# Kernel tuning notes

Hardware: AMD Instinct MI355X
Metric: run time of the kernel (lower is better)

The kernel has to match this reference:

```python
import jax, jax.numpy as jnp
import numpy as np

B, N, LAT, H, NL, NH = 1, 512, 128, 256, 3, 4
EMB = H // 4  # atom-type embedding dim = 64
DH = H // NH  # head dim = 64
LN_EPS = 1e-5


def _lin(x, w, b):
    # torch nn.Linear convention: w is (out, in)
    return x @ w.T + b


def _ln(x, s, b):
    m = jnp.mean(x, -1, keepdims=True)
    v = jnp.mean((x - m) ** 2, -1, keepdims=True)
    return (x - m) / jnp.sqrt(v + LN_EPS) * s + b


def setup_inputs() -> dict:
    key = jax.random.key(0)
    ks = iter(jax.random.split(key, 64))
    def w(shape, scale=0.02):
        return (jax.random.normal(next(ks), shape, jnp.float32) * scale).astype(jnp.float32)
    inp = dict(
        z=jax.random.normal(next(ks), (B, N, LAT), jnp.float32),
        z_global=jax.random.normal(next(ks), (B, LAT), jnp.float32),
        atom_types=jax.random.randint(next(ks), (B, N), 0, 4),
        emb=w((4, EMB), 1.0),
        ip_w1=w((H, LAT + EMB)), ip_b1=jnp.zeros(H), ip_w2=w((H, H)), ip_b2=jnp.zeros(H),
        gp_w1=w((H, LAT)), gp_b1=jnp.zeros(H), gp_w2=w((H, H)), gp_b2=jnp.zeros(H),
        tf_wqkv=w((NL, 3 * H, H)), tf_bqkv=jnp.zeros((NL, 3 * H)),
        tf_wo=w((NL, H, H)), tf_bo=jnp.zeros((NL, H)),
        tf_ln1_s=jnp.ones((NL, H)), tf_ln1_b=jnp.zeros((NL, H)),
        tf_w1=w((NL, 4 * H, H)), tf_b1=jnp.zeros((NL, 4 * H)),
        tf_w2=w((NL, H, 4 * H)), tf_b2=jnp.zeros((NL, H)),
        tf_ln2_s=jnp.ones((NL, H)), tf_ln2_b=jnp.zeros((NL, H)),
        dp_w1=w((H, 2 * H)), dp_b1=jnp.zeros(H), dp_w2=w((H, H)), dp_b2=jnp.zeros(H),
        dp_w3=w((1, H)), dp_b3=jnp.zeros(1),
        cp_w1=w((H, H)), cp_b1=jnp.zeros(H), cp_w2=w((3, H)), cp_b2=jnp.zeros(3),
    )
    return inp


def _forward(z, z_global, atom_types, emb,
             ip_w1, ip_b1, ip_w2, ip_b2,
             gp_w1, gp_b1, gp_w2, gp_b2,
             tf_wqkv, tf_bqkv, tf_wo, tf_bo, tf_ln1_s, tf_ln1_b,
             tf_w1, tf_b1, tf_w2, tf_b2, tf_ln2_s, tf_ln2_b,
             dp_w1, dp_b1, dp_w2, dp_b2, dp_w3, dp_b3,
             cp_w1, cp_b1, cp_w2, cp_b2):
    Bs, Ns = z.shape[0], z.shape[1]
    atom_feats = emb[atom_types]                      # (B,N,EMB)
    z_input = jnp.concatenate([z, atom_feats], -1)    # (B,N,LAT+EMB)
    h = _lin(jax.nn.silu(_lin(z_input, ip_w1, ip_b1)), ip_w2, ip_b2)
    g = _lin(jax.nn.silu(_lin(z_global, gp_w1, gp_b1)), gp_w2, gp_b2)
    h = h + g[:, None, :]
    # post-norm TransformerEncoder (relu FFN, eval mode -> no dropout)
    scale = 1.0 / np.sqrt(DH)
    for l in range(NL):
        qkv = _lin(h, tf_wqkv[l], tf_bqkv[l])
        q, k, v = jnp.split(qkv, 3, -1)
        q = q.reshape(Bs, Ns, NH, DH)
        k = k.reshape(Bs, Ns, NH, DH)
        v = v.reshape(Bs, Ns, NH, DH)
        att = jax.nn.softmax(jnp.einsum('bqhd,bkhd->bhqk', q, k) * scale, -1)
        o = jnp.einsum('bhqk,bkhd->bqhd', att, v).reshape(Bs, Ns, H)
        h = _ln(h + _lin(o, tf_wo[l], tf_bo[l]), tf_ln1_s[l], tf_ln1_b[l])
        ff = _lin(jax.nn.relu(_lin(h, tf_w1[l], tf_b1[l])), tf_w2[l], tf_b2[l])
        h = _ln(h + ff, tf_ln2_s[l], tf_ln2_b[l])
    # dist head: Linear(concat(h_i,h_j)) == h_i @ W[:, :H].T + h_j @ W[:, H:].T + b
    # (avoids materializing the (B,N,N,2H) concat; identical math)
    ai = h @ dp_w1[:, :H].T                           # (B,N,H)
    aj = h @ dp_w1[:, H:].T                           # (B,N,H)
    pair = jax.nn.silu(ai[:, :, None, :] + aj[:, None, :, :] + dp_b1)  # (B,N,N,H)
    pair = jax.nn.silu(_lin(pair, dp_w2, dp_b2))
    dist = jax.nn.softplus(_lin(pair, dp_w3, dp_b3))[..., 0]           # (B,N,N)
    dist = (dist + jnp.swapaxes(dist, 1, 2)) * 0.5
    x = _lin(jax.nn.silu(_lin(h, cp_w1, cp_b1)), cp_w2, cp_b2)          # (B,N,3)
    return x, dist


def reference(z, z_global, atom_types, emb,
              ip_w1, ip_b1, ip_w2, ip_b2,
              gp_w1, gp_b1, gp_w2, gp_b2,
              tf_wqkv, tf_bqkv, tf_wo, tf_bo, tf_ln1_s, tf_ln1_b,
              tf_w1, tf_b1, tf_w2, tf_b2, tf_ln2_s, tf_ln2_b,
              dp_w1, dp_b1, dp_w2, dp_b2, dp_w3, dp_b3,
              cp_w1, cp_b1, cp_w2, cp_b2):
    return _forward(z, z_global, atom_types, emb,
                    ip_w1, ip_b1, ip_w2, ip_b2,
                    gp_w1, gp_b1, gp_w2, gp_b2,
                    tf_wqkv, tf_bqkv, tf_wo, tf_bo, tf_ln1_s, tf_ln1_b,
                    tf_w1, tf_b1, tf_w2, tf_b2, tf_ln2_s, tf_ln2_b,
                    dp_w1, dp_b1, dp_w2, dp_b2, dp_w3, dp_b3,
                    cp_w1, cp_b1, cp_w2, cp_b2)
```

## Files before the change

kernel.cpp:

```cpp
#include <hip/hip_runtime.h>
#include <hip/hip_bf16.h>
#include <cstdint>

typedef __bf16 bf16;
typedef __attribute__((ext_vector_type(8))) __bf16 bf16x8;
typedef __attribute__((ext_vector_type(4))) float f32x4;

#define MFMA16(a, b, c) __builtin_amdgcn_mfma_f32_16x16x32_bf16(a, b, c, 0, 0, 0)

__device__ __forceinline__ float fast_rcp(float x) { return __builtin_amdgcn_rcpf(x); }
__device__ __forceinline__ float silu_f(float x) { return x * fast_rcp(1.f + __expf(-x)); }
__device__ __forceinline__ bf16x8 cvt8(float4 a, float4 b) {
  bf16x8 o;
  o[0]=(bf16)a.x; o[1]=(bf16)a.y; o[2]=(bf16)a.z; o[3]=(bf16)a.w;
  o[4]=(bf16)b.x; o[5]=(bf16)b.y; o[6]=(bf16)b.z; o[7]=(bf16)b.w;
  return o;
}

constexpr long WB_IPW1 = 0;
constexpr long WB_IPW2 = 49152;
constexpr long WB_QKV  = 114688;
constexpr long WB_WO   = 704512;
constexpr long WB_W1   = 901120;
constexpr long WB_W2   = 1687552;
constexpr long WB_CPW1 = 2670592;
constexpr long F_ZIN = 5472256;
constexpr long F_G   = F_ZIN + 512L*192*4;
constexpr long F_H   = F_G + 1024;
constexpr long F_QKV = F_H + 512L*256*4;
constexpr long F_S   = F_QKV + 512L*768*4;
constexpr long F_VT  = F_S + 4L*512*512*4;
constexpr long F_O   = F_VT + 4L*64*512*2;
constexpr long F_T1  = F_O + 512L*256*4;
constexpr long O_W2P  = F_T1 + 512L*256*4;
constexpr long O_WDP  = O_W2P + 131072;
constexpr long O_B512 = O_WDP + 262144;

__global__ __launch_bounds__(256) void prep_kernel(
    const float* __restrict__ s_ipw1, const float* __restrict__ s_ipw2,
    const float* __restrict__ s_qkv,  const float* __restrict__ s_wo,
    const float* __restrict__ s_w1,   const float* __restrict__ s_w2,
    const float* __restrict__ s_dpw1, const float* __restrict__ s_dpw2,
    const float* __restrict__ s_cpw1, bf16* __restrict__ dst,
    const float* __restrict__ z, const int* __restrict__ at, const float* __restrict__ emb,
    const float* __restrict__ zg, const float* __restrict__ gw1, const float* __restrict__ gb1,
    const float* __restrict__ gw2, const float* __restrict__ gb2,
    const float* __restrict__ dpb1,
    float* __restrict__ zi, bf16* __restrict__ w2p, bf16* __restrict__ wdp,
    float* __restrict__ g, float* __restrict__ bias512)
{
  __shared__ float zs[128];
  __shared__ float ts[256];
  const int b = blockIdx.x, tid = threadIdx.x;
  if (b < 2672) {
    long v = (long)b * 256 + tid;
    if (v >= 684032) return;
    const float* src; long off;
    if (v < 176128) {
      if (v < 12288)      { src = s_ipw1; off = 0; }
      else if (v < 28672) { src = s_ipw2; off = 12288; }
      else                { src = s_qkv;  off = 28672; }
    } else if (v < 618496) {
      if (v < 225280)      { src = s_wo; off = 176128; }
      else if (v < 421888) { src = s_w1; off = 225280; }
      else                 { src = s_w2; off = 421888; }
    } else {
      if (v < 651264)      { src = s_dpw1; off = 618496; }
      else if (v < 667648) { src = s_dpw2; off = 651264; }
      else                 { src = s_cpw1; off = 667648; }
    }
    long e = (v - off) * 4;
    float4 f = *(const float4*)&src[e];
    bf16* d = dst + off * 4 + e;
    d[0] = (bf16)f.x; d[1] = (bf16)f.y; d[2] = (bf16)f.z; d[3] = (bf16)f.w;
  } else if (b < 3056) {
    int idx = (b - 2672) * 256 + tid;
    int n = idx / 192, c = idx - n * 192;
    zi[idx] = (c < 128) ? z[n * 128 + c] : emb[at[n] * 64 + (c - 128)];
  } else if (b < 3088) {
    int f = (b - 3056) * 256 + tid;
    int l15 = f & 15, kq = (f >> 4) & 3, ks = (f >> 6) & 7, nt = f >> 9;
    int n = nt * 16 + l15, k0 = ks * 32 + kq * 8;
    float4 v0 = *(const float4*)&s_dpw2[n * 256 + k0];
    float4 v1 = *(const float4*)&s_dpw2[n * 256 + k0 + 4];
    *(bf16x8*)&w2p[(long)f * 8] = cvt8(v0, v1);
  } else if (b < 3216) {
    int v = (b - 3088) * 256 + tid;
    int r = v >> 6, c4 = (v & 63) << 2;
    long src = (r < 256) ? ((long)r * 512 + c4) : ((long)(r - 256) * 512 + 256 + c4);
    float4 f = *(const float4*)&s_dpw1[src];
    bf16* d = &wdp[r * 256 + c4];
    d[0]=(bf16)f.x; d[1]=(bf16)f.y; d[2]=(bf16)f.z; d[3]=(bf16)f.w;
  } else if (b == 3216) {
    if (tid < 128) zs[tid] = zg[tid];
    __syncthreads();
    float s = gb1[tid];
    for (int k = 0; k < 128; ++k) s += zs[k] * gw1[tid * 128 + k];
    ts[tid] = silu_f(s);
    __syncthreads();
    float s2 = gb2[tid];
    for (int k = 0; k < 256; ++k) s2 += ts[k] * gw2[tid * 256 + k];
    g[tid] = s2;
  } else {
    bias512[tid] = dpb1[tid];
    bias512[256 + tid] = 0.f;
  }
}

template<int ACT, typename WT>
__global__ __launch_bounds__(256) void gemm_kernel(
    const float* __restrict__ A, int lda, long sA,
    const WT* __restrict__ W, int ldw, long sW,
    const float* __restrict__ bias,
    const float* __restrict__ R, int ldr, long sR,
    float* __restrict__ C, int ldc, long sC, int K)
{
  const int bz = blockIdx.z;
  A += (long)bz * sA;  W += (long)bz * sW;  C += (long)bz * sC;
  if (R) R += (long)bz * sR;
  const int m0 = blockIdx.x * 64, n0 = blockIdx.y * 64;
  __shared__ bf16 As[64][72];
  __shared__ bf16 Ws[64][72];
  const int tid = threadIdx.x;
  const int lane = tid & 63, wid = tid >> 6;
  const int wm = (wid & 1) * 32, wn = (wid >> 1) * 32;
  const int rr = lane & 15, kg = (lane >> 4) << 3;
  f32x4 acc[2][2] = {};

  float4 rA[4];
  float4 rWf[4];
  uint2  rWh[4];

  auto load_tile = [&](int k0) {
#pragma unroll
    for (int r = 0; r < 4; ++r) {
      int lin = tid + r * 256;
      int row = lin >> 4, kc = (lin & 15) << 2;
      rA[r] = *(const float4*)&A[(long)(m0 + row) * lda + k0 + kc];
      if constexpr (sizeof(WT) == 4)
        rWf[r] = *(const float4*)&W[(long)(n0 + row) * ldw + k0 + kc];
      else
        rWh[r] = *(const uint2*)&W[(long)(n0 + row) * ldw + k0 + kc];
    }
  };
  auto store_tile = [&]() {
#pragma unroll
    for (int r = 0; r < 4; ++r) {
      int lin = tid + r * 256;
      int row = lin >> 4, kc = (lin & 15) << 2;
      As[row][kc] = (bf16)rA[r].x; As[row][kc + 1] = (bf16)rA[r].y;
      As[row][kc + 2] = (bf16)rA[r].z; As[row][kc + 3] = (bf16)rA[r].w;
      if constexpr (sizeof(WT) == 4) {
        Ws[row][kc] = (bf16)rWf[r].x; Ws[row][kc + 1] = (bf16)rWf[r].y;
        Ws[row][kc + 2] = (bf16)rWf[r].z; Ws[row][kc + 3] = (bf16)rWf[r].w;
      } else {
        *(uint2*)&Ws[row][kc] = rWh[r];
      }
    }
  };
  auto do_mfma = [&]() {
#pragma unroll
    for (int ks = 0; ks < 2; ++ks) {
      const int kk = ks * 32 + kg;
      bf16x8 a0 = *(const bf16x8*)&As[wm + rr][kk];
      bf16x8 a1 = *(const bf16x8*)&As[wm + 16 + rr][kk];
      bf16x8 b0 = *(const bf16x8*)&Ws[wn + rr][kk];
      bf16x8 b1 = *(const bf16x8*)&Ws[wn + 16 + rr][kk];
      acc[0][0] = MFMA16(a0, b0, acc[0][0]);
      acc[0][1] = MFMA16(a0, b1, acc[0][1]);
      acc[1][0] = MFMA16(a1, b0, acc[1][0]);
      acc[1][1] = MFMA16(a1, b1, acc[1][1]);
    }
  };

  load_tile(0);
  store_tile();
  __syncthreads();
  for (int k0 = 64; k0 < K; k0 += 64) {
    load_tile(k0);
    do_mfma();
    __syncthreads();
    store_tile();
    __syncthreads();
  }
  do_mfma();

  const int rg = lane >> 4;
#pragma unroll
  for (int mi = 0; mi < 2; ++mi)
#pragma unroll
    for (int ni = 0; ni < 2; ++ni)
#pragma unroll
      for (int r = 0; r < 4; ++r) {
        int gm = m0 + wm + mi * 16 + rg * 4 + r;
        int gn = n0 + wn + ni * 16 + rr;
        float v = acc[mi][ni][r];
        if (bias) v += bias[gn];
        if (R) v += R[(long)gm * ldr + gn];
        if (ACT == 1) v = silu_f(v);
        else if (ACT == 2) v = fmaxf(v, 0.f);
        C[(long)gm * ldc + gn] = v;
      }
}

__global__ __launch_bounds__(256) void softvt_kernel(
    float* __restrict__ S, const float* __restrict__ qkv, bf16* __restrict__ vt)
{
  const int b = blockIdx.x, tid = threadIdx.x;
  if (b < 2048) {
    float* row = S + (long)b * 512;
    float a = row[tid] * 0.125f, e1v = row[tid + 256] * 0.125f;
    float m = fmaxf(a, e1v);
#pragma unroll
    for (int o = 1; o < 64; o <<= 1) m = fmaxf(m, __shfl_xor(m, o));
    __shared__ float red[4];
    __shared__ float red2[4];
    int wid = tid >> 6;
    if ((tid & 63) == 0) red[wid] = m;
    __syncthreads();
    m = fmaxf(fmaxf(red[0], red[1]), fmaxf(red[2], red[3]));
    float e0 = __expf(a - m), e1 = __expf(e1v - m);
    float s = e0 + e1;
#pragma unroll
    for (int o = 1; o < 64; o <<= 1) s += __shfl_xor(s, o);
    if ((tid & 63) == 0) red2[wid] = s;
    __syncthreads();
    s = red2[0] + red2[1] + red2[2] + red2[3];
    float inv = fast_rcp(s);
    row[tid] = e0 * inv; row[tid + 256] = e1 * inv;
  } else {
    int idx = (b - 2048) * 256 + tid;
    int hh = idx >> 15;
    int r = idx & 32767;
    int d = r >> 9, n = r & 511;
    vt[idx] = (bf16)qkv[(long)n * 768 + 512 + hh * 64 + d];
  }
}

__global__ __launch_bounds__(256) void ln_kernel(
    const float* __restrict__ X, const float* __restrict__ sc,
    const float* __restrict__ bi, float* __restrict__ Y)
{
  int row = blockIdx.x, tid = threadIdx.x;
  float v = X[(long)row * 256 + tid];
  float s = v;
#pragma unroll
  for (int o = 1; o < 64; o <<= 1) s += __shfl_xor(s, o);
  __shared__ float r1[4];
  __shared__ float r2[4];
  if ((tid & 63) == 0) r1[tid >> 6] = s;
  __syncthreads();
  float mean = (r1[0] + r1[1] + r1[2] + r1[3]) * (1.f / 256.f);
  float d = v - mean;
  float t = d * d;
#pragma unroll
  for (int o = 1; o < 64; o <<= 1) t += __shfl_xor(t, o);
  if ((tid & 63) == 0) r2[tid >> 6] = t;
  __syncthreads();
  float var = (r2[0] + r2[1] + r2[2] + r2[3]) * (1.f / 256.f);
  Y[(long)row * 256 + tid] = d * rsqrtf(var + 1e-5f) * sc[tid] + bi[tid];
}

#define P2_BUILD(CIDX, TBUF)                                                     \
  {                                                                              \
    const int j0b = jbase + (CIDX) * 32;                                         \
    const float* ajp = aj + (long)(j0b + pp) * 512;                              \
    _Pragma("unroll")                                                            \
    for (int r = 0; r < 4; ++r) {                                                \
      int kk = kb + 8 * r;                                                       \
      float4 a0 = *(const float4*)(ajp + kk * 8);                                \
      float4 a1 = *(const float4*)(ajp + kk * 8 + 4);                            \
      const float* aip = ai_s + kk * 8;                                          \
      bf16x8 tv;                                                                 \
      tv[0] = (bf16)silu_f(a0.x + aip[0]); tv[1] = (bf16)silu_f(a0.y + aip[1]);  \
      tv[2] = (bf16)silu_f(a0.z + aip[2]); tv[3] = (bf16)silu_f(a0.w + aip[3]);  \
      tv[4] = (bf16)silu_f(a1.x + aip[4]); tv[5] = (bf16)silu_f(a1.y + aip[5]);  \
      tv[6] = (bf16)silu_f(a1.z + aip[6]); tv[7] = (bf16)silu_f(a1.w + aip[7]);  \
      *(bf16x8*)&TBUF[(kk * 32 + pp) * 8] = tv;                                  \
    }                                                                            \
  }

#define P2_MFMA(TBUF, ACC)                                                       \
  _Pragma("unroll")                                                              \
  for (int ks = 0; ks < 8; ++ks) {                                               \
    bf16x8 af0 = *(const bf16x8*)&TBUF[((ks * 4 + kq) * 32 + l15) * 8];          \
    bf16x8 af1 = *(const bf16x8*)&TBUF[((ks * 4 + kq) * 32 + 16 + l15) * 8];     \
    _Pragma("unroll")                                                            \
    for (int nt = 0; nt < 4; ++nt) {                                             \
      bf16x8 bfv = *(const bf16x8*)(w2base + (long)(nt * 8 + ks) * 512);         \
      ACC[0][nt] = MFMA16(af0, bfv, ACC[0][nt]);                                 \
      ACC[1][nt] = MFMA16(af1, bfv, ACC[1][nt]);                                 \
    }                                                                            \
  }

#define P2_EPI(ACC, PBUF)                                                        \
  _Pragma("unroll")                                                              \
  for (int Mt = 0; Mt < 2; ++Mt)                                                 \
    _Pragma("unroll")                                                            \
    for (int r = 0; r < 4; ++r) {                                                \
      float s = silu_f(ACC[Mt][0][r] + b2v[0]) * w3v[0]                          \
              + silu_f(ACC[Mt][1][r] + b2v[1]) * w3v[1]                          \
              + silu_f(ACC[Mt][2][r] + b2v[2]) * w3v[2]                          \
              + silu_f(ACC[Mt][3][r] + b2v[3]) * w3v[3];                         \
      s += __shfl_xor(s, 1); s += __shfl_xor(s, 2);                              \
      s += __shfl_xor(s, 4); s += __shfl_xor(s, 8);                              \
      if (l15 == 0) PBUF[Mt * 16 + kq * 4 + r][w] = s;                           \
    }

#define P2_DIST(CIDX, PBUF)                                                      \
  if (tid < 32) {                                                                \
    float s = PBUF[tid][0] + PBUF[tid][1] + PBUF[tid][2] + PBUF[tid][3] + b3v;   \
    float dd = fmaxf(s, 0.f) + log1pf(__expf(-fabsf(s)));                        \
    dout[(long)i * 512 + jbase + (CIDX) * 32 + tid] = dd;                        \
  }

__global__ __launch_bounds__(256, 2) void pair2_kernel(
    const float* __restrict__ ai, const float* __restrict__ aj,
    const bf16* __restrict__ W2P, const float* __restrict__ b2g,
    const float* __restrict__ w3g, const float* __restrict__ b3p,
    float* __restrict__ dout)
{
  __shared__ float ai_s[256];
  __shared__ bf16 t0_s[32 * 256];
  __shared__ bf16 t1_s[32 * 256];
  __shared__ float p0_s[32][4];
  __shared__ float p1_s[32][4];
  const int tid = threadIdx.x, lane = tid & 63, w = tid >> 6;
  const int l15 = lane & 15, kq = lane >> 4;
  const int pp = tid & 31, kb = tid >> 5;
  const int i = blockIdx.x >> 1, half = blockIdx.x & 1;
  const int jbase = half * 256;
  const float b3v = b3p[0];

  ai_s[tid] = ai[(long)i * 512 + tid];

  float b2v[4], w3v[4];
#pragma unroll
  for (int nt = 0; nt < 4; ++nt) {
    int ntg = w * 4 + nt;
    b2v[nt] = b2g[ntg * 16 + l15];
    w3v[nt] = w3g[ntg * 16 + l15];
  }
  const bf16* w2base = W2P + ((long)((w * 128 + kq) * 16 + l15)) * 8;
  __syncthreads();

  P2_BUILD(0, t0_s);
  __syncthreads();
#pragma unroll 1
  for (int cp = 0; cp < 4; ++cp) {
    const int c0 = cp * 2, c1 = cp * 2 + 1;
    {
      f32x4 acc[2][4] = {};
      P2_MFMA(t0_s, acc);
      P2_BUILD(c1, t1_s);
      P2_EPI(acc, p0_s);
    }
    __syncthreads();
    P2_DIST(c0, p0_s);
    {
      f32x4 acc[2][4] = {};
      P2_MFMA(t1_s, acc);
      if (cp < 3) P2_BUILD(c1 + 1, t0_s);
      P2_EPI(acc, p1_s);
    }
    __syncthreads();
    P2_DIST(c1, p1_s);
  }
}

__global__ __launch_bounds__(256) void sym_kernel(float* __restrict__ dist)
{
  int idx = blockIdx.x * 256 + threadIdx.x;
  int i = idx >> 9, j = idx & 511;
  if (i < j) {
    float a = dist[idx];
    float b = dist[(long)j * 512 + i];
    float m = 0.5f * (a + b);
    dist[idx] = m;
    dist[(long)j * 512 + i] = m;
  }
}

__global__ __launch_bounds__(256) void coord_kernel(
    const float* __restrict__ ct, const float* __restrict__ w2,
    const float* __restrict__ b2, float* __restrict__ out)
{
  int t = blockIdx.x * 256 + threadIdx.x;
  if (t >= 1536) return;
  int row = t / 3, c = t - row * 3;
  float s = b2[c];
  const float* a = &ct[(long)row * 256];
  const float* wp = &w2[c * 256];
  for (int k = 0; k < 256; ++k) s += a[k] * wp[k];
  out[t] = s;
}

extern "C" void kernel_launch(void* const* d_in, const int* in_sizes, int n_in,
                              void* d_out, int out_size, void* d_ws, size_t ws_size,
                              hipStream_t stream) {
  const float* z        = (const float*)d_in[0];
  const float* z_global = (const float*)d_in[1];
  const int*   atom_t   = (const int*)d_in[2];
  const float* emb      = (const float*)d_in[3];
  const float* ip_w1 = (const float*)d_in[4];  const float* ip_b1 = (const float*)d_in[5];
  const float* ip_w2 = (const float*)d_in[6];  const float* ip_b2 = (const float*)d_in[7];
  const float* gp_w1 = (const float*)d_in[8];  const float* gp_b1 = (const float*)d_in[9];
  const float* gp_w2 = (const float*)d_in[10]; const float* gp_b2 = (const float*)d_in[11];
  const float* wqkv  = (const float*)d_in[12]; const float* bqkv  = (const float*)d_in[13];
  const float* wo    = (const float*)d_in[14]; const float* bo    = (const float*)d_in[15];
  const float* ln1s  = (const float*)d_in[16]; const float* ln1b  = (const float*)d_in[17];
  const float* w1    = (const float*)d_in[18]; const float* b1    = (const float*)d_in[19];
  const float* w2    = (const float*)d_in[20]; const float* b2    = (const float*)d_in[21];
  const float* ln2s  = (const float*)d_in[22]; const float* ln2b  = (const float*)d_in[23];
  const float* dpw1  = (const float*)d_in[24]; const float* dpb1  = (const float*)d_in[25];
  const float* dpw2  = (const float*)d_in[26]; const float* dpb2  = (const float*)d_in[27];
  const float* dpw3  = (const float*)d_in[28]; const float* dpb3  = (const float*)d_in[29];
  const float* cpw1  = (const float*)d_in[30]; const float* cpb1  = (const float*)d_in[31];
  const float* cpw2  = (const float*)d_in[32]; const float* cpb2  = (const float*)d_in[33];

  char* ws = (char*)d_ws;
  bf16*  WB   = (bf16*)ws;
  float* zin  = (float*)(ws + F_ZIN);
  float* g    = (float*)(ws + F_G);
  float* h    = (float*)(ws + F_H);
  float* qkv  = (float*)(ws + F_QKV);
  float* S    = (float*)(ws + F_S);
  bf16*  Vt   = (bf16*)(ws + F_VT);
  float* o    = (float*)(ws + F_O);
  float* t1   = (float*)(ws + F_T1);
  bf16*  W2P  = (bf16*)(ws + O_W2P);
  bf16*  WDP  = (bf16*)(ws + O_WDP);
  float* b512 = (float*)(ws + O_B512);
  float* ff1  = S;
  float* aiaj = S;
  float* out  = (float*)d_out;
  float* xout = out;
  float* dist = out + 1536;

  prep_kernel<<<3218, 256, 0, stream>>>(ip_w1, ip_w2, wqkv, wo, w1, w2, dpw1, dpw2, cpw1, WB,
      z, atom_t, emb, z_global, gp_w1, gp_b1, gp_w2, gp_b2, dpb1,
      zin, W2P, WDP, g, b512);

  gemm_kernel<1, bf16><<<dim3(8, 4, 1), 256, 0, stream>>>(zin, 192, 0, WB + WB_IPW1, 192, 0,
      ip_b1, nullptr, 0, 0, t1, 256, 0, 192);
  gemm_kernel<0, bf16><<<dim3(8, 4, 1), 256, 0, stream>>>(t1, 256, 0, WB + WB_IPW2, 256, 0,
      ip_b2, g, 0, 0, h, 256, 0, 256);

  for (int l = 0; l < 3; ++l) {
    const bf16* wq = WB + WB_QKV + (long)l * 768 * 256;
    gemm_kernel<0, bf16><<<dim3(8, 12, 1), 256, 0, stream>>>(h, 256, 0, wq, 256, 0,
        bqkv + l * 768, nullptr, 0, 0, qkv, 768, 0, 256);
    gemm_kernel<0, float><<<dim3(8, 8, 4), 256, 0, stream>>>(qkv, 768, 64, qkv + 256, 768, 64,
        nullptr, nullptr, 0, 0, S, 512, 262144, 64);
    softvt_kernel<<<2560, 256, 0, stream>>>(S, qkv, Vt);
    gemm_kernel<0, bf16><<<dim3(8, 1, 4), 256, 0, stream>>>(S, 512, 262144, Vt, 512, 32768,
        nullptr, nullptr, 0, 0, o, 256, 64, 512);
    gemm_kernel<0, bf16><<<dim3(8, 4, 1), 256, 0, stream>>>(o, 256, 0,
        WB + WB_WO + (long)l * 65536, 256, 0, bo + l * 256, h, 256, 0, t1, 256, 0, 256);
    ln_kernel<<<512, 256, 0, stream>>>(t1, ln1s + l * 256, ln1b + l * 256, h);
    gemm_kernel<2, bf16><<<dim3(8, 16, 1), 256, 0, stream>>>(h, 256, 0,
        WB + WB_W1 + (long)l * 262144, 256, 0, b1 + l * 1024, nullptr, 0, 0, ff1, 1024, 0, 256);
    gemm_kernel<0, bf16><<<dim3(8, 4, 1), 256, 0, stream>>>(ff1, 1024, 0,
        WB + WB_W2 + (long)l * 262144, 1024, 0, b2 + l * 256, h, 256, 0, t1, 256, 0, 1024);
    ln_kernel<<<512, 256, 0, stream>>>(t1, ln2s + l * 256, ln2b + l * 256, h);
  }

  gemm_kernel<0, bf16><<<dim3(8, 8, 1), 256, 0, stream>>>(h, 256, 0, WDP, 256, 0,
      b512, nullptr, 0, 0, aiaj, 512, 0, 256);
  pair2_kernel<<<1024, 256, 0, stream>>>(aiaj, aiaj + 256, W2P, dpb2, dpw3, dpb3, dist);
  sym_kernel<<<1024, 256, 0, stream>>>(dist);
  gemm_kernel<1, bf16><<<dim3(8, 4, 1), 256, 0, stream>>>(h, 256, 0, WB + WB_CPW1, 256, 0,
      cpb1, nullptr, 0, 0, t1, 256, 0, 256);
  coord_kernel<<<6, 256, 0, stream>>>(t1, cpw2, cpb2, xout);
}
```

Baseline: 327.7 us.

## Fuse attention stages and merge tail GEMMs and sym/coord kernels

```diff
diff --git a/kernel.cpp b/kernel.cpp
--- a/kernel.cpp
+++ b/kernel.cpp
@@ -203,38 +203,109 @@
       }
 }
 
-__global__ __launch_bounds__(256) void softvt_kernel(
-    float* __restrict__ S, const float* __restrict__ qkv, bf16* __restrict__ vt)
-{
+__global__ __launch_bounds__(256) void qkvt_kernel(
+    const float* __restrict__ qkv, float* __restrict__ S, bf16* __restrict__ vt)
+{
+  __shared__ bf16 As[64][72];
+  __shared__ bf16 Ws[64][72];
   const int b = blockIdx.x, tid = threadIdx.x;
-  if (b < 2048) {
-    float* row = S + (long)b * 512;
-    float a = row[tid] * 0.125f, e1v = row[tid + 256] * 0.125f;
-    float m = fmaxf(a, e1v);
-#pragma unroll
-    for (int o = 1; o < 64; o <<= 1) m = fmaxf(m, __shfl_xor(m, o));
-    __shared__ float red[4];
-    __shared__ float red2[4];
-    int wid = tid >> 6;
-    if ((tid & 63) == 0) red[wid] = m;
-    __syncthreads();
-    m = fmaxf(fmaxf(red[0], red[1]), fmaxf(red[2], red[3]));
-    float e0 = __expf(a - m), e1 = __expf(e1v - m);
-    float s = e0 + e1;
-#pragma unroll
-    for (int o = 1; o < 64; o <<= 1) s += __shfl_xor(s, o);
-    if ((tid & 63) == 0) red2[wid] = s;
-    __syncthreads();
-    s = red2[0] + red2[1] + red2[2] + red2[3];
-    float inv = fast_rcp(s);
-    row[tid] = e0 * inv; row[tid + 256] = e1 * inv;
-  } else {
-    int idx = (b - 2048) * 256 + tid;
+  if (b >= 256) {
+    int idx = (b - 256) * 256 + tid;
     int hh = idx >> 15;
     int r = idx & 32767;
     int d = r >> 9, n = r & 511;
     vt[idx] = (bf16)qkv[(long)n * 768 + 512 + hh * 64 + d];
-  }
+    return;
+  }
+  const int h = b >> 6, m0 = (b & 7) * 64, n0 = ((b >> 3) & 7) * 64;
+  const float* A = qkv + h * 64;
+  const float* W = qkv + 256 + h * 64;
+  float* C = S + (long)h * 262144;
+  const int lane = tid & 63, wid = tid >> 6;
+  const int wm = (wid & 1) * 32, wn = (wid >> 1) * 32;
+  const int rr = lane & 15, kg = (lane >> 4) << 3;
+#pragma unroll
+  for (int r = 0; r < 4; ++r) {
+    int lin = tid + r * 256;
+    int row = lin >> 4, kc = (lin & 15) << 2;
+    float4 va = *(const float4*)&A[(long)(m0 + row) * 768 + kc];
+    As[row][kc] = (bf16)va.x; As[row][kc + 1] = (bf16)va.y;
+    As[row][kc + 2] = (bf16)va.z; As[row][kc + 3] = (bf16)va.w;
+    float4 vw = *(const float4*)&W[(long)(n0 + row) * 768 + kc];
+    Ws[row][kc] = (bf16)vw.x; Ws[row][kc + 1] = (bf16)vw.y;
+    Ws[row][kc + 2] = (bf16)vw.z; Ws[row][kc + 3] = (bf16)vw.w;
+  }
+  __syncthreads();
+  f32x4 acc[2][2] = {};
+#pragma unroll
+  for (int ks = 0; ks < 2; ++ks) {
+    const int kk = ks * 32 + kg;
+    bf16x8 a0 = *(const bf16x8*)&As[wm + rr][kk];
+    bf16x8 a1 = *(const bf16x8*)&As[wm + 16 + rr][kk];
+    bf16x8 b0 = *(const bf16x8*)&Ws[wn + rr][kk];
+    bf16x8 b1 = *(const bf16x8*)&Ws[wn + 16 + rr][kk];
+    acc[0][0] = MFMA16(a0, b0, acc[0][0]);
+    acc[0][1] = MFMA16(a0, b1, acc[0][1]);
+    acc[1][0] = MFMA16(a1, b0, acc[1][0]);
+    acc[1][1] = MFMA16(a1, b1, acc[1][1]);
+  }
+  const int rg = lane >> 4;
+#pragma unroll
+  for (int mi = 0; mi < 2; ++mi)
+#pragma unroll
+    for (int ni = 0; ni < 2; ++ni)
+#pragma unroll
+      for (int r = 0; r < 4; ++r) {
+        int gm = m0 + wm + mi * 16 + rg * 4 + r;
+        int gn = n0 + wn + ni * 16 + rr;
+        C[(long)gm * 512 + gn] = acc[mi][ni][r];
+      }
+}
+
+__global__ __launch_bounds__(256) void softmax_pv_kernel(
+    const float* __restrict__ S, const bf16* __restrict__ Vt, float* __restrict__ o)
+{
+  const int row = blockIdx.x, h = blockIdx.y;
+  const float* srow = S + ((long)h * 512 + row) * 512;
+  __shared__ float p_s[512];
+  __shared__ float red[4];
+  __shared__ float red2[4];
+  __shared__ float part[64][4];
+  const int tid = threadIdx.x;
+  float a = srow[tid] * 0.125f, b = srow[tid + 256] * 0.125f;
+  float m = fmaxf(a, b);
+#pragma unroll
+  for (int t = 1; t < 64; t <<= 1) m = fmaxf(m, __shfl_xor(m, t));
+  int wid = tid >> 6;
+  if ((tid & 63) == 0) red[wid] = m;
+  __syncthreads();
+  m = fmaxf(fmaxf(red[0], red[1]), fmaxf(red[2], red[3]));
+  float e0 = __expf(a - m), e1 = __expf(b - m);
+  float s = e0 + e1;
+#pragma unroll
+  for (int t = 1; t < 64; t <<= 1) s += __shfl_xor(s, t);
+  if ((tid & 63) == 0) red2[wid] = s;
+  __syncthreads();
+  s = red2[0] + red2[1] + red2[2] + red2[3];
+  float inv = fast_rcp(s);
+  p_s[tid] = e0 * inv; p_s[tid + 256] = e1 * inv;
+  __syncthreads();
+  const int d = tid & 63, kc = tid >> 6;
+  const bf16* vp = Vt + (long)h * 32768 + (long)d * 512 + kc * 128;
+  const float* pp = &p_s[kc * 128];
+  float acc = 0.f;
+#pragma unroll
+  for (int k = 0; k < 128; k += 8) {
+    bf16x8 vv = *(const bf16x8*)&vp[k];
+    acc += pp[k]     * (float)vv[0] + pp[k + 1] * (float)vv[1]
+         + pp[k + 2] * (float)vv[2] + pp[k + 3] * (float)vv[3]
+         + pp[k + 4] * (float)vv[4] + pp[k + 5] * (float)vv[5]
+         + pp[k + 6] * (float)vv[6] + pp[k + 7] * (float)vv[7];
+  }
+  part[d][kc] = acc;
+  __syncthreads();
+  if (tid < 64)
+    o[(long)row * 256 + h * 64 + tid] = part[tid][0] + part[tid][1] + part[tid][2] + part[tid][3];
 }
 
 __global__ __launch_bounds__(256) void ln_kernel(
@@ -259,6 +330,84 @@
   __syncthreads();
   float var = (r2[0] + r2[1] + r2[2] + r2[3]) * (1.f / 256.f);
   Y[(long)row * 256 + tid] = d * rsqrtf(var + 1e-5f) * sc[tid] + bi[tid];
+}
+
+__global__ __launch_bounds__(256) void tail_kernel(
+    const float* __restrict__ hsrc,
+    const bf16* __restrict__ WDP, const float* __restrict__ b512, float* __restrict__ aiaj,
+    const bf16* __restrict__ Wcp, const float* __restrict__ cpb1, float* __restrict__ ct)
+{
+  const int y = blockIdx.y;
+  const bf16* W; const float* bias; float* C; int ldc, n0; bool act;
+  if (y < 8) { W = WDP; bias = b512; C = aiaj; ldc = 512; n0 = y * 64; act = false; }
+  else       { W = Wcp; bias = cpb1; C = ct;   ldc = 256; n0 = (y - 8) * 64; act = true; }
+  const int m0 = blockIdx.x * 64;
+  __shared__ bf16 As[64][72];
+  __shared__ bf16 Ws[64][72];
+  const int tid = threadIdx.x;
+  const int lane = tid & 63, wid = tid >> 6;
+  const int wm = (wid & 1) * 32, wn = (wid >> 1) * 32;
+  const int rr = lane & 15, kg = (lane >> 4) << 3;
+  f32x4 acc[2][2] = {};
+  float4 rA[4];
+  uint2  rWh[4];
+  auto load_tile = [&](int k0) {
+#pragma unroll
+    for (int r = 0; r < 4; ++r) {
+      int lin = tid + r * 256;
+      int row = lin >> 4, kc = (lin & 15) << 2;
+      rA[r] = *(const float4*)&hsrc[(long)(m0 + row) * 256 + k0 + kc];
+      rWh[r] = *(const uint2*)&W[(long)(n0 + row) * 256 + k0 + kc];
+    }
+  };
+  auto store_tile = [&]() {
+#pragma unroll
+    for (int r = 0; r < 4; ++r) {
+      int lin = tid + r * 256;
+      int row = lin >> 4, kc = (lin & 15) << 2;
+      As[row][kc] = (bf16)rA[r].x; As[row][kc + 1] = (bf16)rA[r].y;
+      As[row][kc + 2] = (bf16)rA[r].z; As[row][kc + 3] = (bf16)rA[r].w;
+      *(uint2*)&Ws[row][kc] = rWh[r];
+    }
+  };
+  auto do_mfma = [&]() {
+#pragma unroll
+    for (int ks = 0; ks < 2; ++ks) {
+      const int kk = ks * 32 + kg;
+      bf16x8 a0 = *(const bf16x8*)&As[wm + rr][kk];
+      bf16x8 a1 = *(const bf16x8*)&As[wm + 16 + rr][kk];
+      bf16x8 b0 = *(const bf16x8*)&Ws[wn + rr][kk];
+      bf16x8 b1 = *(const bf16x8*)&Ws[wn + 16 + rr][kk];
+      acc[0][0] = MFMA16(a0, b0, acc[0][0]);
+      acc[0][1] = MFMA16(a0, b1, acc[0][1]);
+      acc[1][0] = MFMA16(a1, b0, acc[1][0]);
+      acc[1][1] = MFMA16(a1, b1, acc[1][1]);
+    }
+  };
+  load_tile(0);
+  store_tile();
+  __syncthreads();
+  for (int k0 = 64; k0 < 256; k0 += 64) {
+    load_tile(k0);
+    do_mfma();
+    __syncthreads();
+    store_tile();
+    __syncthreads();
+  }
+  do_mfma();
+  const int rg = lane >> 4;
+#pragma unroll
+  for (int mi = 0; mi < 2; ++mi)
+#pragma unroll
+    for (int ni = 0; ni < 2; ++ni)
+#pragma unroll
+      for (int r = 0; r < 4; ++r) {
+        int gm = m0 + wm + mi * 16 + rg * 4 + r;
+        int gn = n0 + wn + ni * 16 + rr;
+        float v = acc[mi][ni][r] + bias[gn];
+        if (act) v = silu_f(v);
+        C[(long)gm * ldc + gn] = v;
+      }
 }
 
 #define P2_BUILD(CIDX, TBUF)                                                     \
@@ -368,31 +517,32 @@
   }
 }
 
-__global__ __launch_bounds__(256) void sym_kernel(float* __restrict__ dist)
-{
-  int idx = blockIdx.x * 256 + threadIdx.x;
-  int i = idx >> 9, j = idx & 511;
-  if (i < j) {
-    float a = dist[idx];
-    float b = dist[(long)j * 512 + i];
-    float m = 0.5f * (a + b);
-    dist[idx] = m;
-    dist[(long)j * 512 + i] = m;
-  }
-}
-
-__global__ __launch_bounds__(256) void coord_kernel(
+__global__ __launch_bounds__(256) void symcoord_kernel(
+    float* __restrict__ dist,
     const float* __restrict__ ct, const float* __restrict__ w2,
     const float* __restrict__ b2, float* __restrict__ out)
 {
-  int t = blockIdx.x * 256 + threadIdx.x;
-  if (t >= 1536) return;
-  int row = t / 3, c = t - row * 3;
-  float s = b2[c];
-  const float* a = &ct[(long)row * 256];
-  const float* wp = &w2[c * 256];
-  for (int k = 0; k < 256; ++k) s += a[k] * wp[k];
-  out[t] = s;
+  const int b = blockIdx.x, tid = threadIdx.x;
+  if (b < 1024) {
+    int idx = b * 256 + tid;
+    int i = idx >> 9, j = idx & 511;
+    if (i < j) {
+      float a = dist[idx];
+      float bb = dist[(long)j * 512 + i];
+      float m = 0.5f * (a + bb);
+      dist[idx] = m;
+      dist[(long)j * 512 + i] = m;
+    }
+  } else {
+    int t = (b - 1024) * 256 + tid;
+    if (t >= 1536) return;
+    int row = t / 3, c = t - row * 3;
+    float s = b2[c];
+    const float* a = &ct[(long)row * 256];
+    const float* wp = &w2[c * 256];
+    for (int k = 0; k < 256; ++k) s += a[k] * wp[k];
+    out[t] = s;
+  }
 }
 
 extern "C" void kernel_launch(void* const* d_in, const int* in_sizes, int n_in,
@@ -450,11 +600,8 @@
     const bf16* wq = WB + WB_QKV + (long)l * 768 * 256;
     gemm_kernel<0, bf16><<<dim3(8, 12, 1), 256, 0, stream>>>(h, 256, 0, wq, 256, 0,
         bqkv + l * 768, nullptr, 0, 0, qkv, 768, 0, 256);
-    gemm_kernel<0, float><<<dim3(8, 8, 4), 256, 0, stream>>>(qkv, 768, 64, qkv + 256, 768, 64,
-        nullptr, nullptr, 0, 0, S, 512, 262144, 64);
-    softvt_kernel<<<2560, 256, 0, stream>>>(S, qkv, Vt);
-    gemm_kernel<0, bf16><<<dim3(8, 1, 4), 256, 0, stream>>>(S, 512, 262144, Vt, 512, 32768,
-        nullptr, nullptr, 0, 0, o, 256, 64, 512);
+    qkvt_kernel<<<768, 256, 0, stream>>>(qkv, S, Vt);
+    softmax_pv_kernel<<<dim3(512, 4), 256, 0, stream>>>(S, Vt, o);
     gemm_kernel<0, bf16><<<dim3(8, 4, 1), 256, 0, stream>>>(o, 256, 0,
         WB + WB_WO + (long)l * 65536, 256, 0, bo + l * 256, h, 256, 0, t1, 256, 0, 256);
     ln_kernel<<<512, 256, 0, stream>>>(t1, ln1s + l * 256, ln1b + l * 256, h);
@@ -465,11 +612,8 @@
     ln_kernel<<<512, 256, 0, stream>>>(t1, ln2s + l * 256, ln2b + l * 256, h);
   }
 
-  gemm_kernel<0, bf16><<<dim3(8, 8, 1), 256, 0, stream>>>(h, 256, 0, WDP, 256, 0,
-      b512, nullptr, 0, 0, aiaj, 512, 0, 256);
+  tail_kernel<<<dim3(8, 12), 256, 0, stream>>>(h, WDP, b512, aiaj,
+      WB + WB_CPW1, cpb1, t1);
   pair2_kernel<<<1024, 256, 0, stream>>>(aiaj, aiaj + 256, W2P, dpb2, dpw3, dpb3, dist);
-  sym_kernel<<<1024, 256, 0, stream>>>(dist);
-  gemm_kernel<1, bf16><<<dim3(8, 4, 1), 256, 0, stream>>>(h, 256, 0, WB + WB_CPW1, 256, 0,
-      cpb1, nullptr, 0, 0, t1, 256, 0, 256);
-  coord_kernel<<<6, 256, 0, stream>>>(t1, cpw2, cpb2, xout);
-}
+  symcoord_kernel<<<1030, 256, 0, stream>>>(dist, t1, cpw2, cpb2, xout);
+}
```

New measurement: 333.2 us. About the same (+1.7%).
